# Kernel optimization log

Measured on AMD Instinct MI355X. Metric: run time of the kernel, lower is better.

## Reference

```python
import jax, jax.numpy as jnp
import numpy as np

SEQ, BS, DIM = 2048, 2, 256
G, NQ = 2, 8           # n_keys groups, n_queries total
SUB = NQ // G          # queries per group
EPS = 1e-5


def _ln(x, gamma, beta):
    m = jnp.mean(x, axis=-1, keepdims=True)
    v = jnp.mean(jnp.square(x - m), axis=-1, keepdims=True)
    return (x - m) * jax.lax.rsqrt(v + EPS) * gamma + beta


def setup_inputs() -> dict:
    key = jax.random.key(0)
    ks = jax.random.split(key, 16)
    s = 0.02
    return {
        "x":   jax.random.normal(ks[0], (SEQ, BS, DIM), jnp.float32),
        # block layernorms
        "g0": jnp.ones((DIM,), jnp.float32), "b0": jnp.zeros((DIM,), jnp.float32),
        "g1": jnp.ones((DIM,), jnp.float32), "b1": jnp.zeros((DIM,), jnp.float32),
        # attention q/k layernorm (norm_kvs=True)
        "gn": jnp.ones((DIM,), jnp.float32), "bn": jnp.zeros((DIM,), jnp.float32),
        # attention projections (torch Linear: weight [out,in])
        "wk": jax.random.normal(ks[1], (DIM * G, DIM), jnp.float32) * s,
        "bk": jnp.zeros((DIM * G,), jnp.float32),
        "wv": jax.random.normal(ks[2], (DIM * G, DIM), jnp.float32) * s,
        "bv": jnp.zeros((DIM * G,), jnp.float32),
        "wq": jax.random.normal(ks[3], (DIM * NQ, DIM), jnp.float32) * s,
        "bq": jnp.zeros((DIM * NQ,), jnp.float32),
        "wo": jax.random.normal(ks[4], (DIM, DIM * NQ), jnp.float32) * s,
        "bo": jnp.zeros((DIM,), jnp.float32),
        # FFN: BayesLora(dim,2dim) -> relu -> BayesLora(2dim,dim), eval == plain linear
        "w1": jax.random.normal(ks[5], (2 * DIM, DIM), jnp.float32) * s,
        "bf1": jnp.zeros((2 * DIM,), jnp.float32),
        "w2": jax.random.normal(ks[6], (DIM, 2 * DIM), jnp.float32) * s,
        "bf2": jnp.zeros((DIM,), jnp.float32),
    }


def reference(x, g0, b0, g1, b1, gn, bn, wk, bk, wv, bv, wq, bq, wo, bo, w1, bf1, w2, bf2):
    seq, bs, dim = x.shape
    # --- attention (pre-norm) ---
    h = _ln(x, g0, b0)                                        # s b d
    K = (h @ wk.T + bk).reshape(seq, bs, G, dim)              # s b g i
    V = (h @ wv.T + bv).reshape(seq, bs, G, dim)              # s b g i
    Q = (h @ wq.T + bq).reshape(seq, bs, G, SUB, dim)         # s b g u i
    K = _ln(K, gn, bn)
    Q = _ln(Q, gn, bn)
    scores = jnp.einsum('sbgui,tbgi->bgust', Q, K) / jnp.sqrt(jnp.float32(dim))
    neg = jnp.finfo(scores.dtype).min
    causal = jnp.tril(jnp.ones((seq, seq), bool))             # s1 >= s2 allowed
    scores = jnp.where(causal, scores, neg)
    probs = jax.nn.softmax(scores, axis=-1)                   # b g u s t
    out = jnp.einsum('bgust,tbgi->sbgui', probs, V)
    out = out.reshape(seq, bs, G * SUB * dim)                 # s b (g u i)
    x = x + (out @ wo.T + bo)
    # --- FFN (pre-norm) ---
    h2 = _ln(x, g1, b1)
    f = jax.nn.relu(h2 @ w1.T + bf1) @ w2.T + bf2
    return x + f
```

## Files before the change

### kernel.cpp

```cpp
#include <hip/hip_runtime.h>
#include <hip/hip_bf16.h>

#define SEQ  2048
#define BSZ  2
#define DIM  256
#define NG   2
#define NQH  8
#define SUBQ 4
#define ROWS (SEQ*BSZ)
#define NQKV 3072
#define QROW 6144

typedef unsigned int uint32;
typedef unsigned short ushort;
typedef __attribute__((ext_vector_type(8))) short short8;
typedef __attribute__((ext_vector_type(4))) float f32x4;

__device__ __forceinline__ float bflo(uint32 u){
  union { uint32 i; float f; } c; c.i = u << 16; return c.f;
}
__device__ __forceinline__ float bfhi(uint32 u){
  union { uint32 i; float f; } c; c.i = u & 0xffff0000u; return c.f;
}
__device__ __forceinline__ uint32 pack2(float a, float b){
  __hip_bfloat16 ha = __float2bfloat16(a);
  __hip_bfloat16 hb = __float2bfloat16(b);
  unsigned short ua, ub;
  __builtin_memcpy(&ua, &ha, 2);
  __builtin_memcpy(&ub, &hb, 2);
  return (uint32)ua | ((uint32)ub << 16);
}
__device__ __forceinline__ ushort bf16bits(float v){
  __hip_bfloat16 h = __float2bfloat16(v);
  ushort u; __builtin_memcpy(&u, &h, 2); return u;
}

__device__ __forceinline__ void dma16(const void* g, void* l) {
  __builtin_amdgcn_global_load_lds(
      (const __attribute__((address_space(1))) uint32*)g,
      (__attribute__((address_space(3))) uint32*)l, 16, 0, 0);
}

__global__ __launch_bounds__(256) void wcvt6(
    const float* __restrict__ wk, const float* __restrict__ wv,
    const float* __restrict__ wq, const float* __restrict__ wo,
    const float* __restrict__ w1, const float* __restrict__ w2,
    const float* __restrict__ bk, const float* __restrict__ bv,
    const float* __restrict__ bq,
    __hip_bfloat16* __restrict__ out, float* __restrict__ bc)
{
  int u = blockIdx.x * 256 + threadIdx.x;
  if (u < 196608) {
    int lane = u & 63, col = lane & 15, quad = lane >> 4;
    const float* srcrow;
    if (u < 98304) {
      int n16 = u >> 9, kc = (u >> 6) & 7;
      int n = n16 * 16 + col;
      const float* m = (n < 512) ? (wk + (size_t)n * 256)
                     : (n < 1024) ? (wv + (size_t)(n - 512) * 256)
                                  : (wq + (size_t)(n - 1024) * 256);
      srcrow = m + kc * 32 + quad * 8;
    } else if (u < 163840) {
      int local = u - 98304;
      int n16 = local >> 12, kc = (local >> 6) & 63;
      srcrow = wo + (size_t)(n16 * 16 + col) * 2048 + kc * 32 + quad * 8;
    } else if (u < 180224) {
      int local = u - 163840;
      int n16 = local >> 9, kc = (local >> 6) & 7;
      srcrow = w1 + (size_t)(n16 * 16 + col) * 256 + kc * 32 + quad * 8;
    } else {
      int local = u - 180224;
      int n16 = local >> 10, kc = (local >> 6) & 15;
      srcrow = w2 + (size_t)(n16 * 16 + col) * 512 + kc * 32 + quad * 8;
    }
    float4 a = *(const float4*)srcrow;
    float4 b = *(const float4*)(srcrow + 4);
    uint4 st;
    st.x = pack2(a.x, a.y); st.y = pack2(a.z, a.w);
    st.z = pack2(b.x, b.y); st.w = pack2(b.z, b.w);
    *(uint4*)((ushort*)out + (size_t)u * 8) = st;
  } else {
    int bu = u - 196608;
    const float* src; int loc;
    if      (bu < 128) { src = bk; loc = bu; }
    else if (bu < 256) { src = bv; loc = bu - 128; }
    else               { src = bq; loc = bu - 256; }
    *(float4*)(bc + 4 * (size_t)bu) = *(const float4*)(src + 4 * (size_t)loc);
  }
}

__global__ __launch_bounds__(256) void ln_rows_w(
    const float* __restrict__ in,
    const float* __restrict__ gamma,
    const float* __restrict__ beta,
    __hip_bfloat16* __restrict__ out)
{
  int wave = threadIdx.x >> 6, lane = threadIdx.x & 63;
  int row = blockIdx.x * 4 + wave;
  size_t base = (size_t)row * DIM + lane * 4;
  float4 v = *(const float4*)(in + base);
  float s  = v.x + v.y + v.z + v.w;
  float s2 = v.x*v.x + v.y*v.y + v.z*v.z + v.w*v.w;
  #pragma unroll
  for (int o = 1; o < 64; o <<= 1) {
    s  += __shfl_xor(s, o);
    s2 += __shfl_xor(s2, o);
  }
  float m = s * (1.0f / DIM);
  float rb = rsqrtf(s2 * (1.0f / DIM) - m * m + 1e-5f);
  float4 gm = *(const float4*)(gamma + lane * 4);
  float4 bt = *(const float4*)(beta + lane * 4);
  uint2 st;
  st.x = pack2((v.x - m) * rb * gm.x + bt.x, (v.y - m) * rb * gm.y + bt.y);
  st.y = pack2((v.z - m) * rb * gm.z + bt.z, (v.w - m) * rb * gm.w + bt.w);
  *(uint2*)(out + base) = st;
}

__global__ __launch_bounds__(256) void ln_qkv_w(
    __hip_bfloat16* __restrict__ QKV,
    const float* __restrict__ gamma,
    const float* __restrict__ beta)
{
  int wave = threadIdx.x >> 6, lane = threadIdx.x & 63;
  int idx = blockIdx.x * 4 + wave;
  size_t base;
  if (idx < ROWS * NG) {
    base = (size_t)(idx >> 1) * NQKV + (idx & 1) * DIM;
  } else {
    int j = idx - ROWS * NG;
    base = (size_t)(j >> 3) * NQKV + 2 * NG * DIM + (j & 7) * DIM;
  }
  __hip_bfloat16* p = QKV + base + lane * 4;
  uint2 u = *(const uint2*)p;
  float v0 = bflo(u.x), v1 = bfhi(u.x), v2 = bflo(u.y), v3 = bfhi(u.y);
  float s  = v0 + v1 + v2 + v3;
  float s2 = v0*v0 + v1*v1 + v2*v2 + v3*v3;
  #pragma unroll
  for (int o = 1; o < 64; o <<= 1) {
    s  += __shfl_xor(s, o);
    s2 += __shfl_xor(s2, o);
  }
  float m = s * (1.0f / DIM);
  float rb = rsqrtf(s2 * (1.0f / DIM) - m * m + 1e-5f);
  float4 gm = *(const float4*)(gamma + lane * 4);
  float4 bt = *(const float4*)(beta + lane * 4);
  uint2 st;
  st.x = pack2((v0 - m) * rb * gm.x + bt.x, (v1 - m) * rb * gm.y + bt.y);
  st.y = pack2((v2 - m) * rb * gm.z + bt.z, (v3 - m) * rb * gm.w + bt.w);
  *(uint2*)p = st;
}

__global__ __launch_bounds__(256) void kf_swizzle(
    const __hip_bfloat16* __restrict__ QKV, __hip_bfloat16* __restrict__ Kf)
{
  int wave = threadIdx.x >> 6, lane = threadIdx.x & 63;
  int col = lane & 15, quad = lane >> 4;
  int cid = blockIdx.x * 4 + wave;
  int nk = cid & 15, kt = (cid >> 4) & 63, bg = cid >> 10;
  int b = bg >> 1, g = bg & 1;
  int tc = nk >> 3, ks = nk & 7;
  const ushort* src = (const ushort*)QKV
      + ((size_t)(kt * 32 + tc * 16 + col) * BSZ + b) * NQKV + g * DIM + ks * 32 + quad * 8;
  uint4 v = *(const uint4*)src;
  *(uint4*)((ushort*)Kf + (size_t)cid * 512 + lane * 8) = v;
}

__global__ __launch_bounds__(256) void v_swizzle(
    const __hip_bfloat16* __restrict__ QKV, __hip_bfloat16* __restrict__ Vf)
{
  __shared__ ushort T[64][72];
  int t0 = blockIdx.x * 64, d0 = blockIdx.y * 64, bg = blockIdx.z;
  int b = bg >> 1, g = bg & 1;
  int tid = threadIdx.x;
  int tr = tid >> 2, c4 = (tid & 3) * 16;
  const ushort* src = (const ushort*)QKV + ((size_t)(t0 + tr) * BSZ + b) * NQKV
                    + NG * DIM + g * DIM + d0 + c4;
  uint4 a0 = *(const uint4*)src;
  uint4 a1 = *(const uint4*)(src + 8);
  *(uint4*)&T[tr][c4]     = a0;
  *(uint4*)&T[tr][c4 + 8] = a1;
  __syncthreads();
  #pragma unroll
  for (int k2 = 0; k2 < 2; ++k2) {
    int u = tid * 2 + k2;
    int tt = u >> 8, di = (u >> 6) & 3, qd = (u >> 4) & 3, cl = u & 15;
    ushort tmp[8];
    #pragma unroll
    for (int e = 0; e < 8; ++e) tmp[e] = T[tt * 32 + qd * 8 + e][di * 16 + cl];
    int kt = (t0 >> 5) + tt;
    int dc = (d0 >> 4) + di;
    *(uint4*)((ushort*)Vf + (((size_t)(bg * 64 + kt) * 16 + dc) << 9) + (qd * 16 + cl) * 8)
        = *(uint4*)tmp;
  }
}

template<int GN, int RELU, int OUTMODE>
__global__ __launch_bounds__(256) void gemm_mfma(
    const __hip_bfloat16* __restrict__ A,
    const __hip_bfloat16* __restrict__ W,
    const float* __restrict__ bias,
    const float* __restrict__ resid,
    void* __restrict__ outp,
    int M, int N, int K)
{
  constexpr int WCH = GN / 16;
  constexpr int MC  = (GN == 128) ? 4 : 2;
  __shared__ __align__(16) ushort AS[2][4096];
  __shared__ __align__(16) ushort WS[2][WCH * 512];

  const int tid = threadIdx.x;
  const int wave = tid >> 6, lane = tid & 63;
  const int col = lane & 15, quad = lane >> 4;
  const int wm = (GN == 128) ? (wave >> 1) : wave;
  const int wn = (GN == 128) ? (wave & 1) : 0;
  const int bn0 = blockIdx.x * GN;
  const int bm0 = blockIdx.y * 128;
  const int Keff  = (OUTMODE == 2) ? (K / gridDim.z) : K;
  const int kbase = (OUTMODE == 2) ? blockIdx.z * Keff : 0;
  const int kiters = Keff >> 5;

  f32x4 acc[MC][4];
  #pragma unroll
  for (int mc = 0; mc < MC; ++mc)
    #pragma unroll
    for (int nc = 0; nc < 4; ++nc)
      acc[mc][nc] = (f32x4){0.f, 0.f, 0.f, 0.f};

  auto stage = [&](int it, int bufi) {
    int k0 = kbase + it * 32;
    #pragma unroll
    for (int c = 0; c < 2; ++c) {
      int ch = wave * 2 + c;
      dma16((const ushort*)A + (size_t)(bm0 + ch * 16 + col) * K + k0 + quad * 8,
            &AS[bufi][ch * 512]);
    }
    #pragma unroll
    for (int c = 0; c < WCH / 4; ++c) {
      int ch = wave * (WCH / 4) + c;
      dma16((const ushort*)W + (((size_t)((bn0 >> 4) + ch) * (K >> 5) + (k0 >> 5)) << 9) + lane * 8,
            &WS[bufi][ch * 512]);
    }
  };

  stage(0, 0);
  for (int it = 0; it < kiters; ++it) {
    int cur = it & 1;
    __syncthreads();
    if (it + 1 < kiters) stage(it + 1, 1 - cur);
    short8 af[MC], bf_[4];
    #pragma unroll
    for (int mc = 0; mc < MC; ++mc)
      af[mc] = *(const short8*)&AS[cur][(wm * MC + mc) * 512 + lane * 8];
    #pragma unroll
    for (int nc = 0; nc < 4; ++nc)
      bf_[nc] = *(const short8*)&WS[cur][(wn * 4 + nc) * 512 + lane * 8];
    #pragma unroll
    for (int mc = 0; mc < MC; ++mc)
      #pragma unroll
      for (int nc = 0; nc < 4; ++nc)
        acc[mc][nc] = __builtin_amdgcn_mfma_f32_16x16x32_bf16(af[mc], bf_[nc], acc[mc][nc], 0, 0, 0);
  }

  #pragma unroll
  for (int nc = 0; nc < 4; ++nc) {
    int n = bn0 + wn * 64 + nc * 16 + col;
    float bv = 0.f;
    if (OUTMODE != 2) bv = bias[n];
    #pragma unroll
    for (int mc = 0; mc < MC; ++mc) {
      #pragma unroll
      for (int reg = 0; reg < 4; ++reg) {
        int m = bm0 + wm * (MC * 16) + mc * 16 + quad * 4 + reg;
        float v = acc[mc][nc][reg] + bv;
        if (OUTMODE != 2 && resid) v += resid[(size_t)m * N + n];
        if (RELU) v = fmaxf(v, 0.f);
        if (OUTMODE == 0)
          ((__hip_bfloat16*)outp)[(size_t)m * N + n] = __float2bfloat16(v);
        else if (OUTMODE == 1)
          ((float*)outp)[(size_t)m * N + n] = v;
        else
          ((float*)outp)[(size_t)blockIdx.z * M * N + (size_t)m * N + n] = v;
      }
    }
  }
}

__global__ __launch_bounds__(256) void combine2(
    const float* __restrict__ P, const float* __restrict__ bias,
    const float* __restrict__ resid, float* __restrict__ out, int MN)
{
  int i4 = (blockIdx.x * 256 + threadIdx.x) * 4;
  float4 a = *(const float4*)(P + i4);
  float4 b = *(const float4*)(P + MN + i4);
  float4 r = *(const float4*)(resid + i4);
  float4 bb = *(const float4*)(bias + (i4 & (DIM - 1)));
  float4 o;
  o.x = a.x + b.x + r.x + bb.x;
  o.y = a.y + b.y + r.y + bb.y;
  o.z = a.z + b.z + r.z + bb.z;
  o.w = a.w + b.w + r.w + bb.w;
  *(float4*)(out + i4) = o;
}

__global__ __launch_bounds__(256) void combine_ln2(
    const float* __restrict__ P, const float* __restrict__ bias,
    const float* __restrict__ resid, float* __restrict__ X2,
    const float* __restrict__ gamma, const float* __restrict__ beta,
    __hip_bfloat16* __restrict__ H2)
{
  const int MN = ROWS * DIM;
  int wave = threadIdx.x >> 6, lane = threadIdx.x & 63;
  int row = blockIdx.x * 4 + wave;
  size_t i = (size_t)row * DIM + lane * 4;
  float4 a = *(const float4*)(P + i);
  float4 b = *(const float4*)(P + MN + i);
  float4 r = *(const float4*)(resid + i);
  float4 bb = *(const float4*)(bias + lane * 4);
  float4 v;
  v.x = a.x + b.x + r.x + bb.x;
  v.y = a.y + b.y + r.y + bb.y;
  v.z = a.z + b.z + r.z + bb.z;
  v.w = a.w + b.w + r.w + bb.w;
  *(float4*)(X2 + i) = v;
  float s  = v.x + v.y + v.z + v.w;
  float s2 = v.x*v.x + v.y*v.y + v.z*v.z + v.w*v.w;
  #pragma unroll
  for (int o = 1; o < 64; o <<= 1) {
    s  += __shfl_xor(s, o);
    s2 += __shfl_xor(s2, o);
  }
  float m = s * (1.0f / DIM);
  float rb = rsqrtf(s2 * (1.0f / DIM) - m * m + 1e-5f);
  float4 gm = *(const float4*)(gamma + lane * 4);
  float4 bt = *(const float4*)(beta + lane * 4);
  uint2 st;
  st.x = pack2((v.x - m) * rb * gm.x + bt.x, (v.y - m) * rb * gm.y + bt.y);
  st.y = pack2((v.z - m) * rb * gm.z + bt.z, (v.w - m) * rb * gm.w + bt.w);
  *(uint2*)(H2 + i) = st;
}

__global__ __launch_bounds__(256, 2) void attn_mfma(
    const __hip_bfloat16* __restrict__ QKV,
    const __hip_bfloat16* __restrict__ Kf,
    const __hip_bfloat16* __restrict__ Vf,
    __hip_bfloat16* __restrict__ Ob,
    __hip_bfloat16* __restrict__ Op1,
    float* __restrict__ Lp)
{
  __shared__ __align__(16) ushort KS[2][8192];
  __shared__ __align__(16) ushort VS[2][8192];
  __shared__ __align__(16) ushort Pw[4][1280];

  const int tid  = threadIdx.x;
  const int wave = tid >> 6, lane = tid & 63;
  const int col  = lane & 15, quad = lane >> 4;
  const int head = blockIdx.x & 15;
  const int w    = blockIdx.x >> 4;
  int qb, z, split, nit, k0;
  if (w < 24) { qb = 15 - (w >> 1); z = w & 1; split = 1; nit = 2 * qb + 2; k0 = z * nit; }
  else        { qb = 27 - w;        z = 0;     split = 0; nit = 4 * qb + 4; k0 = 0; }

  const int b = head >> 3, hq = head & 7, g = hq >> 2;
  const int bg = b * NG + g;
  const int qw0 = qb * 128 + wave * 32;

  short8 qf[2][8];
  #pragma unroll
  for (int mc = 0; mc < 2; ++mc) {
    int s = qw0 + mc * 16 + col;
    const ushort* qp = (const ushort*)QKV + (size_t)s * QROW + b * NQKV
                     + 2 * NG * DIM + hq * DIM + quad * 8;
    #pragma unroll
    for (int ks = 0; ks < 8; ++ks)
      qf[mc][ks] = *(const short8*)(qp + ks * 32);
  }

  short8 onesf;
  #pragma unroll
  for (int i = 0; i < 8; ++i) onesf[i] = (short)0x3F80;

  f32x4 o[2][16];
  #pragma unroll
  for (int mc = 0; mc < 2; ++mc)
    #pragma unroll
    for (int dc = 0; dc < 16; ++dc)
      o[mc][dc] = (f32x4){0.f, 0.f, 0.f, 0.f};
  float l_s[2][4] = {{0.f}};

  auto stage = [&](int i, int bufi) {
    int kt = k0 + i;
    const ushort* kb = (const ushort*)Kf + (((size_t)bg * 64 + kt) << 13);
    const ushort* vb = (const ushort*)Vf + (((size_t)bg * 64 + kt) << 13);
    #pragma unroll
    for (int cc = 0; cc < 4; ++cc) {
      int nk = wave * 4 + cc;
      dma16(kb + (nk << 9) + lane * 8, &KS[bufi][nk * 512]);
      dma16(vb + (nk << 9) + lane * 8, &VS[bufi][nk * 512]);
    }
  };

  stage(0, 0);
  for (int i = 0; i < nit; ++i) {
    int cur = i & 1;
    __syncthreads();
    if (i + 1 < nit) stage(i + 1, 1 - cur);
    int kt = k0 + i;
    if (kt * 32 > qw0 + 31) continue;

    f32x4 sf[2][2];
    #pragma unroll
    for (int mc = 0; mc < 2; ++mc)
      #pragma unroll
      for (int tc = 0; tc < 2; ++tc)
        sf[mc][tc] = (f32x4){0.f, 0.f, 0.f, 0.f};
    #pragma unroll
    for (int ks = 0; ks < 8; ++ks) {
      short8 kb0 = *(const short8*)&KS[cur][ks * 512 + lane * 8];
      short8 kb1 = *(const short8*)&KS[cur][(8 + ks) * 512 + lane * 8];
      sf[0][0] = __builtin_amdgcn_mfma_f32_16x16x32_bf16(qf[0][ks], kb0, sf[0][0], 0, 0, 0);
      sf[0][1] = __builtin_amdgcn_mfma_f32_16x16x32_bf16(qf[0][ks], kb1, sf[0][1], 0, 0, 0);
      sf[1][0] = __builtin_amdgcn_mfma_f32_16x16x32_bf16(qf[1][ks], kb0, sf[1][0], 0, 0, 0);
      sf[1][1] = __builtin_amdgcn_mfma_f32_16x16x32_bf16(qf[1][ks], kb1, sf[1][1], 0, 0, 0);
    }

    const bool dm = (kt * 32 + 31) > qw0;
    #pragma unroll
    for (int mc = 0; mc < 2; ++mc)
      #pragma unroll
      for (int tc = 0; tc < 2; ++tc)
        #pragma unroll
        for (int reg = 0; reg < 4; ++reg) {
          float p = __expf(sf[mc][tc][reg] * 0.0625f);
          if (dm) {
            int tg = kt * 32 + tc * 16 + col;
            int sg = qw0 + mc * 16 + quad * 4 + reg;
            if (tg > sg) p = 0.f;
          }
          Pw[wave][(mc * 16 + quad * 4 + reg) * 40 + tc * 16 + col] = bf16bits(p);
        }

    short8 pa0 = *(const short8*)&Pw[wave][col * 40 + quad * 8];
    short8 pa1 = *(const short8*)&Pw[wave][(16 + col) * 40 + quad * 8];

    f32x4 zz = (f32x4){0.f, 0.f, 0.f, 0.f};
    f32x4 ps0 = __builtin_amdgcn_mfma_f32_16x16x32_bf16(pa0, onesf, zz, 0, 0, 0);
    f32x4 ps1 = __builtin_amdgcn_mfma_f32_16x16x32_bf16(pa1, onesf, zz, 0, 0, 0);
    #pragma unroll
    for (int r = 0; r < 4; ++r) { l_s[0][r] += ps0[r]; l_s[1][r] += ps1[r]; }

    #pragma unroll
    for (int dc = 0; dc < 16; ++dc) {
      short8 vb = *(const short8*)&VS[cur][dc * 512 + lane * 8];
      o[0][dc] = __builtin_amdgcn_mfma_f32_16x16x32_bf16(pa0, vb, o[0][dc], 0, 0, 0);
      o[1][dc] = __builtin_amdgcn_mfma_f32_16x16x32_bf16(pa1, vb, o[1][dc], 0, 0, 0);
    }
  }

  if (!split) {
    #pragma unroll
    for (int mc = 0; mc < 2; ++mc)
      #pragma unroll
      for (int reg = 0; reg < 4; ++reg) {
        float inv = 1.0f / l_s[mc][reg];
        int s = qw0 + mc * 16 + quad * 4 + reg;
        __hip_bfloat16* op = Ob + (size_t)s * (BSZ * NQH * DIM) + b * (NQH * DIM) + hq * DIM;
        #pragma unroll
        for (int dc = 0; dc < 16; ++dc)
          op[dc * 16 + col] = __float2bfloat16(o[mc][dc][reg] * inv);
      }
  } else {
    #pragma unroll
    for (int mc = 0; mc < 2; ++mc)
      #pragma unroll
      for (int reg = 0; reg < 4; ++reg) {
        int s = qw0 + mc * 16 + quad * 4 + reg;
        int row = s - 512;
        __hip_bfloat16* op = (z == 0)
            ? Ob  + (size_t)s   * (BSZ * NQH * DIM) + b * (NQH * DIM) + hq * DIM
            : Op1 + (size_t)row * (BSZ * NQH * DIM) + b * (NQH * DIM) + hq * DIM;
        #pragma unroll
        for (int dc = 0; dc < 16; ++dc)
          op[dc * 16 + col] = __float2bfloat16(o[mc][dc][reg]);
        if (col == 0) Lp[(z * 1536 + row) * 16 + head] = l_s[mc][reg];
      }
  }
}

__global__ __launch_bounds__(256) void attn_norm(
    __hip_bfloat16* __restrict__ Ob, const __hip_bfloat16* __restrict__ Op1,
    const float* __restrict__ Lp)
{
  int i4 = (blockIdx.x * 256 + threadIdx.x) * 4;
  int row = i4 >> 12;
  int off = i4 & 4095;
  int head = off >> 8;
  float inv = 1.0f / (Lp[row * 16 + head] + Lp[(1536 + row) * 16 + head]);
  ushort* a = (ushort*)Ob + (size_t)(row + 512) * 4096 + off;
  const ushort* c = (const ushort*)Op1 + (size_t)row * 4096 + off;
  uint2 ua = *(const uint2*)a;
  uint2 uc = *(const uint2*)c;
  uint2 st;
  st.x = pack2((bflo(ua.x) + bflo(uc.x)) * inv, (bfhi(ua.x) + bfhi(uc.x)) * inv);
  st.y = pack2((bflo(ua.y) + bflo(uc.y)) * inv, (bfhi(ua.y) + bfhi(uc.y)) * inv);
  *(uint2*)a = st;
}

extern "C" void kernel_launch(void* const* d_in, const int* in_sizes, int n_in,
                              void* d_out, int out_size, void* d_ws, size_t ws_size,
                              hipStream_t stream)
{
  const float* x   = (const float*)d_in[0];
  const float* g0  = (const float*)d_in[1];
  const float* b0  = (const float*)d_in[2];
  const float* g1  = (const float*)d_in[3];
  const float* b1  = (const float*)d_in[4];
  const float* gn  = (const float*)d_in[5];
  const float* bn  = (const float*)d_in[6];
  const float* wk  = (const float*)d_in[7];
  const float* bk  = (const float*)d_in[8];
  const float* wv  = (const float*)d_in[9];
  const float* bv  = (const float*)d_in[10];
  const float* wq  = (const float*)d_in[11];
  const float* bq  = (const float*)d_in[12];
  const float* wo  = (const float*)d_in[13];
  const float* bo  = (const float*)d_in[14];
  const float* w1  = (const float*)d_in[15];
  const float* bf1 = (const float*)d_in[16];
  const float* w2  = (const float*)d_in[17];
  const float* bf2 = (const float*)d_in[18];

  char* ws = (char*)d_ws;
  const size_t MB = 1024 * 1024;
  __hip_bfloat16* QKV = (__hip_bfloat16*)(ws);
  float*          Pwo = (float*)         (ws);
  float*          X2  = (float*)         (ws + 8  * MB);
  __hip_bfloat16* H2  = (__hip_bfloat16*)(ws + 12 * MB);
  __hip_bfloat16* F1  = (__hip_bfloat16*)(ws + 14 * MB);
  float*          Pw2 = (float*)         (ws + 18 * MB);
  __hip_bfloat16* H   = (__hip_bfloat16*)(ws + 24 * MB);
  __hip_bfloat16* Kf  = (__hip_bfloat16*)(ws + 24 * MB);
  __hip_bfloat16* Vf  = (__hip_bfloat16*)(ws + 28 * MB);
  __hip_bfloat16* AO  = (__hip_bfloat16*)(ws + 32 * MB);
  __hip_bfloat16* Op1 = (__hip_bfloat16*)(ws + 48 * MB);
  float*          BC  = (float*)         (ws + 60 * MB + 768 * 1024);
  float*          Lp  = (float*)         (ws + 60 * MB + 800 * 1024);
  __hip_bfloat16* WB  = (__hip_bfloat16*)(ws + 61 * MB);

  __hip_bfloat16* woB = WB + 786432;
  __hip_bfloat16* w1B = WB + 1310720;
  __hip_bfloat16* w2B = WB + 1441792;

  wcvt6<<<771, 256, 0, stream>>>(wk, wv, wq, wo, w1, w2, bk, bv, bq, WB, BC);
  ln_rows_w<<<ROWS / 4, 256, 0, stream>>>(x, g0, b0, H);
  gemm_mfma<128,0,0><<<dim3(NQKV/128, ROWS/128), 256, 0, stream>>>(H, WB, BC, nullptr, QKV, ROWS, NQKV, DIM);
  ln_qkv_w<<<(ROWS * NG + ROWS * NQH) / 4, 256, 0, stream>>>(QKV, gn, bn);
  kf_swizzle<<<1024, 256, 0, stream>>>(QKV, Kf);
  v_swizzle<<<dim3(SEQ/64, DIM/64, BSZ*NG), 256, 0, stream>>>(QKV, Vf);
  attn_mfma<<<448, 256, 0, stream>>>(QKV, Kf, Vf, AO, Op1, Lp);
  attn_norm<<<6144, 256, 0, stream>>>(AO, Op1, Lp);
  gemm_mfma<64,0,2><<<dim3(DIM/64, ROWS/128, 2), 256, 0, stream>>>(AO, woB, nullptr, nullptr, Pwo, ROWS, DIM, NQH*DIM);
  combine_ln2<<<ROWS / 4, 256, 0, stream>>>(Pwo, bo, x, X2, g1, b1, H2);
  gemm_mfma<64,1,0><<<dim3((2*DIM)/64, ROWS/128), 256, 0, stream>>>(H2, w1B, bf1, nullptr, F1, ROWS, 2*DIM, DIM);
  gemm_mfma<64,0,2><<<dim3(DIM/64, ROWS/128, 2), 256, 0, stream>>>(F1, w2B, nullptr, nullptr, Pw2, ROWS, DIM, 2*DIM);
  combine2<<<ROWS*DIM/1024, 256, 0, stream>>>(Pw2, bf2, X2, (float*)d_out, ROWS*DIM);
}
```

Baseline: 259.1 us.

## Fuse prep kernels, write LN outputs in MFMA fragment layout, widen Wo split-K

Merges the weight conversion with the first layernorm, and merges the Q/K layernorm, the K swizzle and the V swizzle into one launch. This removes three kernel launches and a separate pass over K. The LN outputs H and H2 are now written directly in the MFMA fragment layout, so the GEMM can load A tiles as contiguous 1 KB chunks. Split-K for the Wo projection goes from 2 to 4, and the combine step now sums four partials. The cost is larger workspace partials and reshuffled buffer offsets, which could alias.

After: 249.3 us. -3.8%, faster.

```diff
diff --git a/kernel.cpp b/kernel.cpp
--- a/kernel.cpp
+++ b/kernel.cpp
@@ -41,160 +41,153 @@
       (__attribute__((address_space(3))) uint32*)l, 16, 0, 0);
 }
 
-__global__ __launch_bounds__(256) void wcvt6(
+__global__ __launch_bounds__(256) void misc0(
     const float* __restrict__ wk, const float* __restrict__ wv,
     const float* __restrict__ wq, const float* __restrict__ wo,
     const float* __restrict__ w1, const float* __restrict__ w2,
     const float* __restrict__ bk, const float* __restrict__ bv,
     const float* __restrict__ bq,
-    __hip_bfloat16* __restrict__ out, float* __restrict__ bc)
-{
-  int u = blockIdx.x * 256 + threadIdx.x;
-  if (u < 196608) {
-    int lane = u & 63, col = lane & 15, quad = lane >> 4;
-    const float* srcrow;
-    if (u < 98304) {
-      int n16 = u >> 9, kc = (u >> 6) & 7;
-      int n = n16 * 16 + col;
-      const float* m = (n < 512) ? (wk + (size_t)n * 256)
-                     : (n < 1024) ? (wv + (size_t)(n - 512) * 256)
-                                  : (wq + (size_t)(n - 1024) * 256);
-      srcrow = m + kc * 32 + quad * 8;
-    } else if (u < 163840) {
-      int local = u - 98304;
-      int n16 = local >> 12, kc = (local >> 6) & 63;
-      srcrow = wo + (size_t)(n16 * 16 + col) * 2048 + kc * 32 + quad * 8;
-    } else if (u < 180224) {
-      int local = u - 163840;
-      int n16 = local >> 9, kc = (local >> 6) & 7;
-      srcrow = w1 + (size_t)(n16 * 16 + col) * 256 + kc * 32 + quad * 8;
+    __hip_bfloat16* __restrict__ out, float* __restrict__ bc,
+    const float* __restrict__ x, const float* __restrict__ g0,
+    const float* __restrict__ b0, __hip_bfloat16* __restrict__ Hf)
+{
+  if (blockIdx.x < 771) {
+    int u = blockIdx.x * 256 + threadIdx.x;
+    if (u < 196608) {
+      int lane = u & 63, col = lane & 15, quad = lane >> 4;
+      const float* srcrow;
+      if (u < 98304) {
+        int n16 = u >> 9, kc = (u >> 6) & 7;
+        int n = n16 * 16 + col;
+        const float* m = (n < 512) ? (wk + (size_t)n * 256)
+                       : (n < 1024) ? (wv + (size_t)(n - 512) * 256)
+                                    : (wq + (size_t)(n - 1024) * 256);
+        srcrow = m + kc * 32 + quad * 8;
+      } else if (u < 163840) {
+        int local = u - 98304;
+        int n16 = local >> 12, kc = (local >> 6) & 63;
+        srcrow = wo + (size_t)(n16 * 16 + col) * 2048 + kc * 32 + quad * 8;
+      } else if (u < 180224) {
+        int local = u - 163840;
+        int n16 = local >> 9, kc = (local >> 6) & 7;
+        srcrow = w1 + (size_t)(n16 * 16 + col) * 256 + kc * 32 + quad * 8;
+      } else {
+        int local = u - 180224;
+        int n16 = local >> 10, kc = (local >> 6) & 15;
+        srcrow = w2 + (size_t)(n16 * 16 + col) * 512 + kc * 32 + quad * 8;
+      }
+      float4 a = *(const float4*)srcrow;
+      float4 b = *(const float4*)(srcrow + 4);
+      uint4 st;
+      st.x = pack2(a.x, a.y); st.y = pack2(a.z, a.w);
+      st.z = pack2(b.x, b.y); st.w = pack2(b.z, b.w);
+      *(uint4*)((ushort*)out + (size_t)u * 8) = st;
     } else {
-      int local = u - 180224;
-      int n16 = local >> 10, kc = (local >> 6) & 15;
-      srcrow = w2 + (size_t)(n16 * 16 + col) * 512 + kc * 32 + quad * 8;
-    }
-    float4 a = *(const float4*)srcrow;
-    float4 b = *(const float4*)(srcrow + 4);
-    uint4 st;
-    st.x = pack2(a.x, a.y); st.y = pack2(a.z, a.w);
-    st.z = pack2(b.x, b.y); st.w = pack2(b.z, b.w);
-    *(uint4*)((ushort*)out + (size_t)u * 8) = st;
+      int bu = u - 196608;
+      const float* src; int loc;
+      if      (bu < 128) { src = bk; loc = bu; }
+      else if (bu < 256) { src = bv; loc = bu - 128; }
+      else               { src = bq; loc = bu - 256; }
+      *(float4*)(bc + 4 * (size_t)bu) = *(const float4*)(src + 4 * (size_t)loc);
+    }
   } else {
-    int bu = u - 196608;
-    const float* src; int loc;
-    if      (bu < 128) { src = bk; loc = bu; }
-    else if (bu < 256) { src = bv; loc = bu - 128; }
-    else               { src = bq; loc = bu - 256; }
-    *(float4*)(bc + 4 * (size_t)bu) = *(const float4*)(src + 4 * (size_t)loc);
-  }
-}
-
-__global__ __launch_bounds__(256) void ln_rows_w(
-    const float* __restrict__ in,
-    const float* __restrict__ gamma,
-    const float* __restrict__ beta,
-    __hip_bfloat16* __restrict__ out)
-{
-  int wave = threadIdx.x >> 6, lane = threadIdx.x & 63;
-  int row = blockIdx.x * 4 + wave;
-  size_t base = (size_t)row * DIM + lane * 4;
-  float4 v = *(const float4*)(in + base);
-  float s  = v.x + v.y + v.z + v.w;
-  float s2 = v.x*v.x + v.y*v.y + v.z*v.z + v.w*v.w;
-  #pragma unroll
-  for (int o = 1; o < 64; o <<= 1) {
-    s  += __shfl_xor(s, o);
-    s2 += __shfl_xor(s2, o);
-  }
-  float m = s * (1.0f / DIM);
-  float rb = rsqrtf(s2 * (1.0f / DIM) - m * m + 1e-5f);
-  float4 gm = *(const float4*)(gamma + lane * 4);
-  float4 bt = *(const float4*)(beta + lane * 4);
-  uint2 st;
-  st.x = pack2((v.x - m) * rb * gm.x + bt.x, (v.y - m) * rb * gm.y + bt.y);
-  st.y = pack2((v.z - m) * rb * gm.z + bt.z, (v.w - m) * rb * gm.w + bt.w);
-  *(uint2*)(out + base) = st;
-}
-
-__global__ __launch_bounds__(256) void ln_qkv_w(
+    int wave = threadIdx.x >> 6, lane = threadIdx.x & 63;
+    int row = (blockIdx.x - 771) * 4 + wave;
+    size_t base = (size_t)row * DIM + lane * 4;
+    float4 v = *(const float4*)(x + base);
+    float s  = v.x + v.y + v.z + v.w;
+    float s2 = v.x*v.x + v.y*v.y + v.z*v.z + v.w*v.w;
+    #pragma unroll
+    for (int o = 1; o < 64; o <<= 1) {
+      s  += __shfl_xor(s, o);
+      s2 += __shfl_xor(s2, o);
+    }
+    float m = s * (1.0f / DIM);
+    float rb = rsqrtf(s2 * (1.0f / DIM) - m * m + 1e-5f);
+    float4 gm = *(const float4*)(g0 + lane * 4);
+    float4 bt = *(const float4*)(b0 + lane * 4);
+    uint2 st;
+    st.x = pack2((v.x - m) * rb * gm.x + bt.x, (v.y - m) * rb * gm.y + bt.y);
+    st.y = pack2((v.z - m) * rb * gm.z + bt.z, (v.w - m) * rb * gm.w + bt.w);
+    int kc = lane >> 3, quad = (lane >> 1) & 3, jj = 4 * (lane & 1);
+    int cid = (row >> 4) * 8 + kc;
+    *(uint2*)((ushort*)Hf + (size_t)cid * 512 + (quad * 16 + (row & 15)) * 8 + jj) = st;
+  }
+}
+
+__global__ __launch_bounds__(256) void ln_swz(
     __hip_bfloat16* __restrict__ QKV,
-    const float* __restrict__ gamma,
-    const float* __restrict__ beta)
-{
-  int wave = threadIdx.x >> 6, lane = threadIdx.x & 63;
-  int idx = blockIdx.x * 4 + wave;
-  size_t base;
-  if (idx < ROWS * NG) {
-    base = (size_t)(idx >> 1) * NQKV + (idx & 1) * DIM;
+    const float* __restrict__ gamma, const float* __restrict__ beta,
+    __hip_bfloat16* __restrict__ Kf, __hip_bfloat16* __restrict__ Vf)
+{
+  int j = blockIdx.x;
+  if (j < 10240) {
+    int wave = threadIdx.x >> 6, lane = threadIdx.x & 63;
+    int idx = j * 4 + wave;
+    size_t base;
+    if (idx < 8192) base = (size_t)(idx >> 1) * NQKV + (idx & 1) * DIM;
+    else {
+      int qi = idx - 8192;
+      base = (size_t)(qi >> 3) * NQKV + 2 * NG * DIM + (qi & 7) * DIM;
+    }
+    __hip_bfloat16* p = QKV + base + lane * 4;
+    uint2 u = *(const uint2*)p;
+    float v0 = bflo(u.x), v1 = bfhi(u.x), v2 = bflo(u.y), v3 = bfhi(u.y);
+    float s  = v0 + v1 + v2 + v3;
+    float s2 = v0*v0 + v1*v1 + v2*v2 + v3*v3;
+    #pragma unroll
+    for (int o = 1; o < 64; o <<= 1) {
+      s  += __shfl_xor(s, o);
+      s2 += __shfl_xor(s2, o);
+    }
+    float m = s * (1.0f / DIM);
+    float rb = rsqrtf(s2 * (1.0f / DIM) - m * m + 1e-5f);
+    float4 gm = *(const float4*)(gamma + lane * 4);
+    float4 bt = *(const float4*)(beta + lane * 4);
+    uint2 st;
+    st.x = pack2((v0 - m) * rb * gm.x + bt.x, (v1 - m) * rb * gm.y + bt.y);
+    st.y = pack2((v2 - m) * rb * gm.z + bt.z, (v3 - m) * rb * gm.w + bt.w);
+    if (idx < 8192) {
+      int r = idx >> 1, gg = idx & 1;
+      int t = r >> 1, b = r & 1;
+      int bg = b * NG + gg;
+      int kt = t >> 5, tr = t & 31, tc = tr >> 4, col = tr & 15;
+      int ks = lane >> 3, quad = (lane >> 1) & 3, jj = 4 * (lane & 1);
+      int cid = (bg * 64 + kt) * 16 + tc * 8 + ks;
+      *(uint2*)((ushort*)Kf + (size_t)cid * 512 + (quad * 16 + col) * 8 + jj) = st;
+    } else {
+      *(uint2*)p = st;
+    }
   } else {
-    int j = idx - ROWS * NG;
-    base = (size_t)(j >> 3) * NQKV + 2 * NG * DIM + (j & 7) * DIM;
-  }
-  __hip_bfloat16* p = QKV + base + lane * 4;
-  uint2 u = *(const uint2*)p;
-  float v0 = bflo(u.x), v1 = bfhi(u.x), v2 = bflo(u.y), v3 = bfhi(u.y);
-  float s  = v0 + v1 + v2 + v3;
-  float s2 = v0*v0 + v1*v1 + v2*v2 + v3*v3;
-  #pragma unroll
-  for (int o = 1; o < 64; o <<= 1) {
-    s  += __shfl_xor(s, o);
-    s2 += __shfl_xor(s2, o);
-  }
-  float m = s * (1.0f / DIM);
-  float rb = rsqrtf(s2 * (1.0f / DIM) - m * m + 1e-5f);
-  float4 gm = *(const float4*)(gamma + lane * 4);
-  float4 bt = *(const float4*)(beta + lane * 4);
-  uint2 st;
-  st.x = pack2((v0 - m) * rb * gm.x + bt.x, (v1 - m) * rb * gm.y + bt.y);
-  st.y = pack2((v2 - m) * rb * gm.z + bt.z, (v3 - m) * rb * gm.w + bt.w);
-  *(uint2*)p = st;
-}
-
-__global__ __launch_bounds__(256) void kf_swizzle(
-    const __hip_bfloat16* __restrict__ QKV, __hip_bfloat16* __restrict__ Kf)
-{
-  int wave = threadIdx.x >> 6, lane = threadIdx.x & 63;
-  int col = lane & 15, quad = lane >> 4;
-  int cid = blockIdx.x * 4 + wave;
-  int nk = cid & 15, kt = (cid >> 4) & 63, bg = cid >> 10;
-  int b = bg >> 1, g = bg & 1;
-  int tc = nk >> 3, ks = nk & 7;
-  const ushort* src = (const ushort*)QKV
-      + ((size_t)(kt * 32 + tc * 16 + col) * BSZ + b) * NQKV + g * DIM + ks * 32 + quad * 8;
-  uint4 v = *(const uint4*)src;
-  *(uint4*)((ushort*)Kf + (size_t)cid * 512 + lane * 8) = v;
-}
-
-__global__ __launch_bounds__(256) void v_swizzle(
-    const __hip_bfloat16* __restrict__ QKV, __hip_bfloat16* __restrict__ Vf)
-{
-  __shared__ ushort T[64][72];
-  int t0 = blockIdx.x * 64, d0 = blockIdx.y * 64, bg = blockIdx.z;
-  int b = bg >> 1, g = bg & 1;
-  int tid = threadIdx.x;
-  int tr = tid >> 2, c4 = (tid & 3) * 16;
-  const ushort* src = (const ushort*)QKV + ((size_t)(t0 + tr) * BSZ + b) * NQKV
-                    + NG * DIM + g * DIM + d0 + c4;
-  uint4 a0 = *(const uint4*)src;
-  uint4 a1 = *(const uint4*)(src + 8);
-  *(uint4*)&T[tr][c4]     = a0;
-  *(uint4*)&T[tr][c4 + 8] = a1;
-  __syncthreads();
-  #pragma unroll
-  for (int k2 = 0; k2 < 2; ++k2) {
-    int u = tid * 2 + k2;
-    int tt = u >> 8, di = (u >> 6) & 3, qd = (u >> 4) & 3, cl = u & 15;
-    ushort tmp[8];
-    #pragma unroll
-    for (int e = 0; e < 8; ++e) tmp[e] = T[tt * 32 + qd * 8 + e][di * 16 + cl];
-    int kt = (t0 >> 5) + tt;
-    int dc = (d0 >> 4) + di;
-    *(uint4*)((ushort*)Vf + (((size_t)(bg * 64 + kt) * 16 + dc) << 9) + (qd * 16 + cl) * 8)
-        = *(uint4*)tmp;
-  }
-}
-
-template<int GN, int RELU, int OUTMODE>
+    __shared__ ushort T[64][72];
+    int vb = j - 10240;
+    int t0 = (vb & 31) * 64, d0 = ((vb >> 5) & 3) * 64, bg = vb >> 7;
+    int b = bg >> 1, g = bg & 1;
+    int tid = threadIdx.x;
+    int tr = tid >> 2, c4 = (tid & 3) * 16;
+    const ushort* src = (const ushort*)QKV + ((size_t)(t0 + tr) * BSZ + b) * NQKV
+                      + NG * DIM + g * DIM + d0 + c4;
+    uint4 a0 = *(const uint4*)src;
+    uint4 a1 = *(const uint4*)(src + 8);
+    *(uint4*)&T[tr][c4]     = a0;
+    *(uint4*)&T[tr][c4 + 8] = a1;
+    __syncthreads();
+    #pragma unroll
+    for (int k2 = 0; k2 < 2; ++k2) {
+      int u = tid * 2 + k2;
+      int tt = u >> 8, di = (u >> 6) & 3, qd = (u >> 4) & 3, cl = u & 15;
+      ushort tmp[8];
+      #pragma unroll
+      for (int e = 0; e < 8; ++e) tmp[e] = T[tt * 32 + qd * 8 + e][di * 16 + cl];
+      int kt = (t0 >> 5) + tt;
+      int dc = (d0 >> 4) + di;
+      *(uint4*)((ushort*)Vf + (((size_t)(bg * 64 + kt) * 16 + dc) << 9) + (qd * 16 + cl) * 8)
+          = *(uint4*)tmp;
+    }
+  }
+}
+
+template<int GN, int RELU, int OUTMODE, int AFRAG>
 __global__ __launch_bounds__(256) void gemm_mfma(
     const __hip_bfloat16* __restrict__ A,
     const __hip_bfloat16* __restrict__ W,
@@ -231,8 +224,12 @@
     #pragma unroll
     for (int c = 0; c < 2; ++c) {
       int ch = wave * 2 + c;
-      dma16((const ushort*)A + (size_t)(bm0 + ch * 16 + col) * K + k0 + quad * 8,
-            &AS[bufi][ch * 512]);
+      if (AFRAG)
+        dma16((const ushort*)A + ((((size_t)(bm0 >> 4) + ch) * (K >> 5) + (k0 >> 5)) << 9) + lane * 8,
+              &AS[bufi][ch * 512]);
+      else
+        dma16((const ushort*)A + (size_t)(bm0 + ch * 16 + col) * K + k0 + quad * 8,
+              &AS[bufi][ch * 512]);
     }
     #pragma unroll
     for (int c = 0; c < WCH / 4; ++c) {
@@ -302,11 +299,11 @@
   *(float4*)(out + i4) = o;
 }
 
-__global__ __launch_bounds__(256) void combine_ln2(
+__global__ __launch_bounds__(256) void combine_ln4(
     const float* __restrict__ P, const float* __restrict__ bias,
     const float* __restrict__ resid, float* __restrict__ X2,
     const float* __restrict__ gamma, const float* __restrict__ beta,
-    __hip_bfloat16* __restrict__ H2)
+    __hip_bfloat16* __restrict__ H2f)
 {
   const int MN = ROWS * DIM;
   int wave = threadIdx.x >> 6, lane = threadIdx.x & 63;
@@ -314,13 +311,15 @@
   size_t i = (size_t)row * DIM + lane * 4;
   float4 a = *(const float4*)(P + i);
   float4 b = *(const float4*)(P + MN + i);
+  float4 c = *(const float4*)(P + 2 * (size_t)MN + i);
+  float4 d = *(const float4*)(P + 3 * (size_t)MN + i);
   float4 r = *(const float4*)(resid + i);
   float4 bb = *(const float4*)(bias + lane * 4);
   float4 v;
-  v.x = a.x + b.x + r.x + bb.x;
-  v.y = a.y + b.y + r.y + bb.y;
-  v.z = a.z + b.z + r.z + bb.z;
-  v.w = a.w + b.w + r.w + bb.w;
+  v.x = a.x + b.x + c.x + d.x + r.x + bb.x;
+  v.y = a.y + b.y + c.y + d.y + r.y + bb.y;
+  v.z = a.z + b.z + c.z + d.z + r.z + bb.z;
+  v.w = a.w + b.w + c.w + d.w + r.w + bb.w;
   *(float4*)(X2 + i) = v;
   float s  = v.x + v.y + v.z + v.w;
   float s2 = v.x*v.x + v.y*v.y + v.z*v.z + v.w*v.w;
@@ -336,7 +335,9 @@
   uint2 st;
   st.x = pack2((v.x - m) * rb * gm.x + bt.x, (v.y - m) * rb * gm.y + bt.y);
   st.y = pack2((v.z - m) * rb * gm.z + bt.z, (v.w - m) * rb * gm.w + bt.w);
-  *(uint2*)(H2 + i) = st;
+  int kc = lane >> 3, quad = (lane >> 1) & 3, jj = 4 * (lane & 1);
+  int cid = (row >> 4) * 8 + kc;
+  *(uint2*)((ushort*)H2f + (size_t)cid * 512 + (quad * 16 + (row & 15)) * 8 + jj) = st;
 }
 
 __global__ __launch_bounds__(256, 2) void attn_mfma(
@@ -533,15 +534,15 @@
   const size_t MB = 1024 * 1024;
   __hip_bfloat16* QKV = (__hip_bfloat16*)(ws);
   float*          Pwo = (float*)         (ws);
-  float*          X2  = (float*)         (ws + 8  * MB);
-  __hip_bfloat16* H2  = (__hip_bfloat16*)(ws + 12 * MB);
-  __hip_bfloat16* F1  = (__hip_bfloat16*)(ws + 14 * MB);
-  float*          Pw2 = (float*)         (ws + 18 * MB);
-  __hip_bfloat16* H   = (__hip_bfloat16*)(ws + 24 * MB);
+  float*          X2  = (float*)         (ws + 16 * MB);
+  __hip_bfloat16* H2f = (__hip_bfloat16*)(ws + 20 * MB);
+  __hip_bfloat16* F1  = (__hip_bfloat16*)(ws + 22 * MB);
+  __hip_bfloat16* Hf  = (__hip_bfloat16*)(ws + 24 * MB);
   __hip_bfloat16* Kf  = (__hip_bfloat16*)(ws + 24 * MB);
   __hip_bfloat16* Vf  = (__hip_bfloat16*)(ws + 28 * MB);
   __hip_bfloat16* AO  = (__hip_bfloat16*)(ws + 32 * MB);
   __hip_bfloat16* Op1 = (__hip_bfloat16*)(ws + 48 * MB);
+  float*          Pw2 = (float*)         (ws + 48 * MB);
   float*          BC  = (float*)         (ws + 60 * MB + 768 * 1024);
   float*          Lp  = (float*)         (ws + 60 * MB + 800 * 1024);
   __hip_bfloat16* WB  = (__hip_bfloat16*)(ws + 61 * MB);
@@ -550,17 +551,14 @@
   __hip_bfloat16* w1B = WB + 1310720;
   __hip_bfloat16* w2B = WB + 1441792;
 
-  wcvt6<<<771, 256, 0, stream>>>(wk, wv, wq, wo, w1, w2, bk, bv, bq, WB, BC);
-  ln_rows_w<<<ROWS / 4, 256, 0, stream>>>(x, g0, b0, H);
-  gemm_mfma<128,0,0><<<dim3(NQKV/128, ROWS/128), 256, 0, stream>>>(H, WB, BC, nullptr, QKV, ROWS, NQKV, DIM);
-  ln_qkv_w<<<(ROWS * NG + ROWS * NQH) / 4, 256, 0, stream>>>(QKV, gn, bn);
-  kf_swizzle<<<1024, 256, 0, stream>>>(QKV, Kf);
-  v_swizzle<<<dim3(SEQ/64, DIM/64, BSZ*NG), 256, 0, stream>>>(QKV, Vf);
+  misc0<<<1795, 256, 0, stream>>>(wk, wv, wq, wo, w1, w2, bk, bv, bq, WB, BC, x, g0, b0, Hf);
+  gemm_mfma<128,0,0,1><<<dim3(NQKV/128, ROWS/128), 256, 0, stream>>>(Hf, WB, BC, nullptr, QKV, ROWS, NQKV, DIM);
+  ln_swz<<<12288, 256, 0, stream>>>(QKV, gn, bn, Kf, Vf);
   attn_mfma<<<448, 256, 0, stream>>>(QKV, Kf, Vf, AO, Op1, Lp);
   attn_norm<<<6144, 256, 0, stream>>>(AO, Op1, Lp);
-  gemm_mfma<64,0,2><<<dim3(DIM/64, ROWS/128, 2), 256, 0, stream>>>(AO, woB, nullptr, nullptr, Pwo, ROWS, DIM, NQH*DIM);
-  combine_ln2<<<ROWS / 4, 256, 0, stream>>>(Pwo, bo, x, X2, g1, b1, H2);
-  gemm_mfma<64,1,0><<<dim3((2*DIM)/64, ROWS/128), 256, 0, stream>>>(H2, w1B, bf1, nullptr, F1, ROWS, 2*DIM, DIM);
-  gemm_mfma<64,0,2><<<dim3(DIM/64, ROWS/128, 2), 256, 0, stream>>>(F1, w2B, nullptr, nullptr, Pw2, ROWS, DIM, 2*DIM);
+  gemm_mfma<64,0,2,0><<<dim3(DIM/64, ROWS/128, 4), 256, 0, stream>>>(AO, woB, nullptr, nullptr, Pwo, ROWS, DIM, NQH*DIM);
+  combine_ln4<<<ROWS / 4, 256, 0, stream>>>(Pwo, bo, x, X2, g1, b1, H2f);
+  gemm_mfma<64,1,0,1><<<dim3((2*DIM)/64, ROWS/128), 256, 0, stream>>>(H2f, w1B, bf1, nullptr, F1, ROWS, 2*DIM, DIM);
+  gemm_mfma<64,0,2,0><<<dim3(DIM/64, ROWS/128, 2), 256, 0, stream>>>(F1, w2B, nullptr, nullptr, Pw2, ROWS, DIM, 2*DIM);
   combine2<<<ROWS*DIM/1024, 256, 0, stream>>>(Pw2, bf2, X2, (float*)d_out, ROWS*DIM);
 }
```
